# Kernel tuning notes

Measured on AMD Instinct MI355X. Metric: run time of the kernel, lower is better.

Reference implementation:

```python
import jax, jax.numpy as jnp
import numpy as np

IN_FEATURES = 4096
OUT_FEATURES = 16384
TOKENS = 8192  # batch 2 * seq 4096, flattened


def setup_inputs() -> dict:
    key = jax.random.key(0)
    k_x, k_w, k_s, k_b = jax.random.split(key, 4)
    x = jax.random.normal(k_x, (TOKENS, IN_FEATURES), dtype=jnp.float32)
    # ternary weights in {-1, 0, +1}, stored as low-precision ints
    weight_ternary = jax.random.randint(k_w, (OUT_FEATURES, IN_FEATURES), 0, 3, dtype=jnp.int32) - 1
    weight_scale = jax.random.uniform(k_s, (1,), dtype=jnp.float32) + 0.5
    bias = jax.random.normal(k_b, (OUT_FEATURES,), dtype=jnp.float32)
    return {"x": x, "weight_ternary": weight_ternary, "weight_scale": weight_scale, "bias": bias}


def reference(x, weight_ternary, weight_scale, bias):
    # forward: out = x @ (ternary.float() * scale).T + bias  (F.linear)
    w_float = weight_ternary.astype(jnp.float32) * weight_scale  # [O, I]
    out = jnp.einsum('ti,oi->to', x, w_float) + bias  # [T, O]
    return out
```

## Files before the change

kernel.cpp:

```cpp
#include <hip/hip_runtime.h>
#include <stdint.h>

#define TOKENS 8192
#define IN_F   4096
#define OUT_F  16384

#define BM 256
#define BN 256
#define BK 128
#define NT (IN_F / BK)

typedef __attribute__((ext_vector_type(4))) float f32x4;
typedef __attribute__((ext_vector_type(4))) int i32x4;


__device__ __forceinline__ int pack4(int a, int b, int c, int d) {
  return (a & 0xff) | ((b & 0xff) << 8) | ((c & 0xff) << 16) | ((d & 0xff) << 24);
}

__global__ void convert_w_i8(const int* __restrict__ w,
                             int8_t* __restrict__ wq, int n16) {
  int stride = gridDim.x * blockDim.x;
  for (int i = blockIdx.x * blockDim.x + threadIdx.x; i < n16; i += stride) {
    i32x4 o;
#pragma unroll
    for (int j = 0; j < 4; ++j) {
      i32x4 a = ((const i32x4*)w)[(size_t)i * 4 + j];
      o[j] = pack4(a.x, a.y, a.z, a.w);
    }
    ((i32x4*)wq)[i] = o;
  }
}

__global__ void convert_x_i8(const float* __restrict__ x,
                             int8_t* __restrict__ xq,
                             float* __restrict__ xs) {
  const int t = blockIdx.x;
  const int tid = threadIdx.x;
  const float* xr = x + (size_t)t * IN_F;

  f32x4 v[4];
  float m = 0.f;
#pragma unroll
  for (int i = 0; i < 4; ++i) {
    v[i] = ((const f32x4*)xr)[tid * 4 + i];
    m = fmaxf(m, fmaxf(fmaxf(fabsf(v[i].x), fabsf(v[i].y)),
                       fmaxf(fabsf(v[i].z), fabsf(v[i].w))));
  }
#pragma unroll
  for (int off = 32; off; off >>= 1) m = fmaxf(m, __shfl_xor(m, off));
  __shared__ float sm[4];
  if ((tid & 63) == 0) sm[tid >> 6] = m;
  __syncthreads();
  m = fmaxf(fmaxf(sm[0], sm[1]), fmaxf(sm[2], sm[3]));

  const float inv = (m > 0.f) ? (127.f / m) : 0.f;
  if (tid == 0) xs[t] = m / 127.f;

  i32x4 o;
#pragma unroll
  for (int i = 0; i < 4; ++i) {
    o[i] = pack4(__float2int_rn(v[i].x * inv), __float2int_rn(v[i].y * inv),
                 __float2int_rn(v[i].z * inv), __float2int_rn(v[i].w * inv));
  }
  ((i32x4*)(xq + (size_t)t * IN_F))[tid] = o;
}


__device__ __forceinline__ void async_lds_16B(const int8_t* g, int8_t* l) {
  __builtin_amdgcn_global_load_lds(
      reinterpret_cast<const __attribute__((address_space(1))) unsigned int*>(
          reinterpret_cast<uintptr_t>(g)),
      reinterpret_cast<__attribute__((address_space(3))) unsigned int*>(
          reinterpret_cast<uintptr_t>(l)),
      16, 0, 0);
}

__global__ __launch_bounds__(512, 2)
void ternary_gemm_i8(const int8_t* __restrict__ A,
                     const int8_t* __restrict__ B,
                     const float* __restrict__ xs,
                     const float* __restrict__ scale_p,
                     const float* __restrict__ bias,
                     float* __restrict__ C) {
  __shared__ __attribute__((aligned(16))) int8_t lds[2][2][BM * BK];

  const int nbn = OUT_F / BN;
  const int cpx = gridDim.x >> 3;
  const int bid = blockIdx.x;
  const int swz = (bid & 7) * cpx + (bid >> 3);
  const int bm = swz / nbn;
  const int bn = swz % nbn;

  const int tid  = threadIdx.x;
  const int lane = tid & 63;
  const int wid  = tid >> 6;
  const int wr   = wid >> 2;
  const int wc   = wid & 3;

  const int r = lane & 15;
  const int g = lane >> 4;
  const int swzr = (r & 7) * 16;

  const int8_t* Ag = A + (size_t)bm * BM * IN_F;
  const int8_t* Bg = B + (size_t)bn * BN * IN_F;

  const int s_rowoff = lane >> 3;
  const int s_colb   = ((lane & 7) ^ (lane >> 3)) * 16;

  auto stage = [&](int8_t* ldsTile, const int8_t* gTile, int half, int kt) {
#pragma unroll
    for (int i = 0; i < 2; ++i) {
      const int rbase = half * 128 + wid * 16 + i * 8;
      const int8_t* src =
          gTile + (size_t)(rbase + s_rowoff) * IN_F + kt * BK + s_colb;
      async_lds_16B(src, ldsTile + rbase * BK);
    }
  };

  i32x4 acc[8][4];
#pragma unroll
  for (int m = 0; m < 8; ++m)
#pragma unroll
    for (int n = 0; n < 4; ++n) acc[m][n] = i32x4{0, 0, 0, 0};

  stage(&lds[0][1][0], Bg, 0, 0);
  stage(&lds[0][1][0], Bg, 1, 0);
  stage(&lds[0][0][0], Ag, 0, 0);
  stage(&lds[0][0][0], Ag, 1, 0);
  stage(&lds[1][1][0], Bg, 0, 1);
  stage(&lds[1][1][0], Bg, 1, 1);
  stage(&lds[1][0][0], Ag, 0, 1);
  asm volatile("s_waitcnt vmcnt(6)" ::: "memory");
  __builtin_amdgcn_s_barrier();

  i32x4 bfr[4][2];
  i32x4 a0[2][2], a1[2][2], a2[2][2], a3[2][2];
#pragma unroll
  for (int n = 0; n < 4; ++n)
#pragma unroll
    for (int ks = 0; ks < 2; ++ks)
      bfr[n][ks] = *(const i32x4*)(&lds[0][1][0] + (wc * 64 + n * 16 + r) * BK +
                                   ((ks * 64 + g * 16) ^ swzr));
#pragma unroll
  for (int m = 0; m < 2; ++m)
#pragma unroll
    for (int ks = 0; ks < 2; ++ks)
      a0[m][ks] = *(const i32x4*)(&lds[0][0][0] + (wr * 128 + m * 16 + r) * BK +
                                  ((ks * 64 + g * 16) ^ swzr));
  asm volatile("s_waitcnt lgkmcnt(0)" ::: "memory");
  __builtin_amdgcn_s_barrier();

  for (int t = 0; t < NT; ++t) {
    const int cur = t & 1;
    const int8_t* Ab = &lds[cur][0][0];
    int8_t* Abw = &lds[cur][0][0];
    int8_t* Bbw = &lds[cur][1][0];
    int8_t* An  = &lds[cur ^ 1][0][0];
    const int8_t* AbN = &lds[cur ^ 1][0][0];
    const int8_t* BbN = &lds[cur ^ 1][1][0];

    __builtin_amdgcn_s_setprio(1);
#pragma unroll
    for (int ks = 0; ks < 2; ++ks)
#pragma unroll
      for (int m = 0; m < 2; ++m)
#pragma unroll
        for (int n = 0; n < 4; ++n)
          acc[m][n] = __builtin_amdgcn_mfma_i32_16x16x64_i8(
              a0[m][ks], bfr[n][ks], acc[m][n], 0, 0, 0);
    __builtin_amdgcn_s_setprio(0);
#pragma unroll
    for (int m = 0; m < 2; ++m)
#pragma unroll
      for (int ks = 0; ks < 2; ++ks)
        a1[m][ks] = *(const i32x4*)(Ab + (wr * 128 + (2 + m) * 16 + r) * BK +
                                    ((ks * 64 + g * 16) ^ swzr));
    if (t + 1 < NT) stage(An, Ag, 1, t + 1);

    __builtin_amdgcn_s_setprio(1);
#pragma unroll
    for (int ks = 0; ks < 2; ++ks)
#pragma unroll
      for (int m = 0; m < 2; ++m)
#pragma unroll
        for (int n = 0; n < 4; ++n)
          acc[2 + m][n] = __builtin_amdgcn_mfma_i32_16x16x64_i8(
              a1[m][ks], bfr[n][ks], acc[2 + m][n], 0, 0, 0);
    __builtin_amdgcn_s_setprio(0);
#pragma unroll
    for (int m = 0; m < 2; ++m)
#pragma unroll
      for (int ks = 0; ks < 2; ++ks)
        a2[m][ks] = *(const i32x4*)(Ab + (wr * 128 + (4 + m) * 16 + r) * BK +
                                    ((ks * 64 + g * 16) ^ swzr));
    if (t + 2 < NT) stage(Bbw, Bg, 0, t + 2);

    __builtin_amdgcn_s_setprio(1);
#pragma unroll
    for (int ks = 0; ks < 2; ++ks)
#pragma unroll
      for (int m = 0; m < 2; ++m)
#pragma unroll
        for (int n = 0; n < 4; ++n)
          acc[4 + m][n] = __builtin_amdgcn_mfma_i32_16x16x64_i8(
              a2[m][ks], bfr[n][ks], acc[4 + m][n], 0, 0, 0);
    __builtin_amdgcn_s_setprio(0);
#pragma unroll
    for (int m = 0; m < 2; ++m)
#pragma unroll
      for (int ks = 0; ks < 2; ++ks)
        a3[m][ks] = *(const i32x4*)(Ab + (wr * 128 + (6 + m) * 16 + r) * BK +
                                    ((ks * 64 + g * 16) ^ swzr));
    if (t + 2 < NT) stage(Bbw, Bg, 1, t + 2);
    asm volatile("s_waitcnt lgkmcnt(0)" ::: "memory");
    __builtin_amdgcn_s_barrier();

    __builtin_amdgcn_s_setprio(1);
#pragma unroll
    for (int ks = 0; ks < 2; ++ks)
#pragma unroll
      for (int m = 0; m < 2; ++m)
#pragma unroll
        for (int n = 0; n < 4; ++n)
          acc[6 + m][n] = __builtin_amdgcn_mfma_i32_16x16x64_i8(
              a3[m][ks], bfr[n][ks], acc[6 + m][n], 0, 0, 0);
    __builtin_amdgcn_s_setprio(0);
    if (t + 2 < NT) {
      stage(Abw, Ag, 0, t + 2);
      asm volatile("s_waitcnt vmcnt(6)" ::: "memory");
    } else {
      asm volatile("s_waitcnt vmcnt(0)" ::: "memory");
    }
    __builtin_amdgcn_s_barrier();
    if (t + 1 < NT) {
#pragma unroll
      for (int n = 0; n < 4; ++n)
#pragma unroll
        for (int ks = 0; ks < 2; ++ks)
          bfr[n][ks] = *(const i32x4*)(BbN + (wc * 64 + n * 16 + r) * BK +
                                       ((ks * 64 + g * 16) ^ swzr));
#pragma unroll
      for (int m = 0; m < 2; ++m)
#pragma unroll
        for (int ks = 0; ks < 2; ++ks)
          a0[m][ks] = *(const i32x4*)(AbN + (wr * 128 + m * 16 + r) * BK +
                                      ((ks * 64 + g * 16) ^ swzr));
      asm volatile("s_waitcnt lgkmcnt(0)" ::: "memory");
    }
    __builtin_amdgcn_s_barrier();
  }

  const float s = scale_p[0];
  const int row0 = bm * BM + wr * 128;
  const int col0 = bn * BN + wc * 64;
  float bv[4];
#pragma unroll
  for (int n = 0; n < 4; ++n) bv[n] = bias[col0 + n * 16 + r];
#pragma unroll
  for (int m = 0; m < 8; ++m) {
#pragma unroll
    for (int j = 0; j < 4; ++j) {
      const int row = row0 + m * 16 + g * 4 + j;
      const float sx = xs[row] * s;
#pragma unroll
      for (int n = 0; n < 4; ++n) {
        const int col = col0 + n * 16 + r;
        C[(size_t)row * OUT_F + col] = (float)acc[m][n][j] * sx + bv[n];
      }
    }
  }
}


__global__ void fallback_kernel(const float* __restrict__ x,
                                const int* __restrict__ w,
                                const float* __restrict__ scale_p,
                                const float* __restrict__ bias,
                                float* __restrict__ out) {
  size_t idx = (size_t)blockIdx.x * 256 + threadIdx.x;
  int t = (int)(idx / OUT_F);
  int o = (int)(idx % OUT_F);
  const float* xr = x + (size_t)t * IN_F;
  const int* wr = w + (size_t)o * IN_F;
  float acc = 0.f;
  for (int k = 0; k < IN_F; ++k) acc += xr[k] * (float)wr[k];
  out[idx] = acc * scale_p[0] + bias[o];
}


extern "C" void kernel_launch(void* const* d_in, const int* in_sizes, int n_in,
                              void* d_out, int out_size, void* d_ws, size_t ws_size,
                              hipStream_t stream) {
  const float* x     = (const float*)d_in[0];
  const int*   w     = (const int*)d_in[1];
  const float* scale = (const float*)d_in[2];
  const float* bias  = (const float*)d_in[3];
  float* out = (float*)d_out;

  const size_t wq_bytes = (size_t)OUT_F * IN_F;
  const size_t xq_bytes = (size_t)TOKENS * IN_F;
  const size_t xs_bytes = (size_t)TOKENS * sizeof(float);

  if (ws_size >= wq_bytes + xq_bytes + xs_bytes) {
    int8_t* wq = (int8_t*)d_ws;
    int8_t* xq = (int8_t*)((char*)d_ws + wq_bytes);
    float*  xs = (float*)((char*)d_ws + wq_bytes + xq_bytes);

    convert_w_i8<<<2048, 256, 0, stream>>>(w, wq, (OUT_F * IN_F) / 16);
    convert_x_i8<<<TOKENS, 256, 0, stream>>>(x, xq, xs);

    dim3 grid((TOKENS / BM) * (OUT_F / BN));
    ternary_gemm_i8<<<grid, 512, 0, stream>>>(xq, wq, xs, scale, bias, out);
  } else {
    size_t total = (size_t)TOKENS * OUT_F;
    fallback_kernel<<<(unsigned)(total / 256), 256, 0, stream>>>(x, w, scale, bias, out);
  }
}
```

Before: 622.6 us.

## Load B fragments directly from global into registers, bypassing LDS

The weight (B) tile is no longer staged through shared memory. Each wave now loads its own B fragments straight from global memory into registers after the last MFMA group of each k-step, and only the activation (A) tile stays double-buffered in LDS. This halves the LDS footprint and removes the B LDS writes and reads. In exchange, the two waves sharing a column slice each fetch the same B data, and the global load latency sits much closer to the point of use.

New measurement: 913.6 us. +46.7%, slower.

```diff
diff --git a/kernel.cpp b/kernel.cpp
--- a/kernel.cpp
+++ b/kernel.cpp
@@ -83,7 +83,7 @@
                      const float* __restrict__ scale_p,
                      const float* __restrict__ bias,
                      float* __restrict__ C) {
-  __shared__ __attribute__((aligned(16))) int8_t lds[2][2][BM * BK];
+  __shared__ __attribute__((aligned(16))) int8_t lds[2][BM * BK];
 
   const int nbn = OUT_F / BN;
   const int cpx = gridDim.x >> 3;
@@ -103,62 +103,62 @@
   const int swzr = (r & 7) * 16;
 
   const int8_t* Ag = A + (size_t)bm * BM * IN_F;
-  const int8_t* Bg = B + (size_t)bn * BN * IN_F;
+  const int8_t* Bg_lane =
+      B + (size_t)(bn * BN + wc * 64 + r) * IN_F + g * 16;
 
   const int s_rowoff = lane >> 3;
   const int s_colb   = ((lane & 7) ^ (lane >> 3)) * 16;
 
-  auto stage = [&](int8_t* ldsTile, const int8_t* gTile, int half, int kt) {
+  auto stageA = [&](int8_t* ldsTile, int half, int kt) {
 #pragma unroll
     for (int i = 0; i < 2; ++i) {
       const int rbase = half * 128 + wid * 16 + i * 8;
       const int8_t* src =
-          gTile + (size_t)(rbase + s_rowoff) * IN_F + kt * BK + s_colb;
+          Ag + (size_t)(rbase + s_rowoff) * IN_F + kt * BK + s_colb;
       async_lds_16B(src, ldsTile + rbase * BK);
     }
   };
 
+  auto loadB = [&](i32x4 (&bf)[4][2], int kt) {
+#pragma unroll
+    for (int n = 0; n < 4; ++n)
+#pragma unroll
+      for (int ks = 0; ks < 2; ++ks)
+        bf[n][ks] = *(const i32x4*)(Bg_lane + (size_t)(n * 16) * IN_F +
+                                    kt * BK + ks * 64);
+  };
+
   i32x4 acc[8][4];
 #pragma unroll
   for (int m = 0; m < 8; ++m)
 #pragma unroll
     for (int n = 0; n < 4; ++n) acc[m][n] = i32x4{0, 0, 0, 0};
-
-  stage(&lds[0][1][0], Bg, 0, 0);
-  stage(&lds[0][1][0], Bg, 1, 0);
-  stage(&lds[0][0][0], Ag, 0, 0);
-  stage(&lds[0][0][0], Ag, 1, 0);
-  stage(&lds[1][1][0], Bg, 0, 1);
-  stage(&lds[1][1][0], Bg, 1, 1);
-  stage(&lds[1][0][0], Ag, 0, 1);
-  asm volatile("s_waitcnt vmcnt(6)" ::: "memory");
-  __builtin_amdgcn_s_barrier();
 
   i32x4 bfr[4][2];
   i32x4 a0[2][2], a1[2][2], a2[2][2], a3[2][2];
-#pragma unroll
-  for (int n = 0; n < 4; ++n)
-#pragma unroll
-    for (int ks = 0; ks < 2; ++ks)
-      bfr[n][ks] = *(const i32x4*)(&lds[0][1][0] + (wc * 64 + n * 16 + r) * BK +
-                                   ((ks * 64 + g * 16) ^ swzr));
+
+  stageA(&lds[0][0], 0, 0);
+  stageA(&lds[0][0], 1, 0);
+  stageA(&lds[1][0], 0, 1);
+  loadB(bfr, 0);
+  asm volatile("s_waitcnt vmcnt(10)" ::: "memory");
+  __builtin_amdgcn_s_barrier();
+
 #pragma unroll
   for (int m = 0; m < 2; ++m)
 #pragma unroll
     for (int ks = 0; ks < 2; ++ks)
-      a0[m][ks] = *(const i32x4*)(&lds[0][0][0] + (wr * 128 + m * 16 + r) * BK +
+      a0[m][ks] = *(const i32x4*)(&lds[0][0] + (wr * 128 + m * 16 + r) * BK +
                                   ((ks * 64 + g * 16) ^ swzr));
   asm volatile("s_waitcnt lgkmcnt(0)" ::: "memory");
   __builtin_amdgcn_s_barrier();
 
   for (int t = 0; t < NT; ++t) {
     const int cur = t & 1;
-    const int8_t* Ab = &lds[cur][0][0];
-    int8_t* Abw = &lds[cur][0][0];
-    int8_t* Bbw = &lds[cur][1][0];
-    int8_t* An  = &lds[cur ^ 1][0][0];
-    const int8_t* AbN = &lds[cur ^ 1][0][0];
-    const int8_t* BbN = &lds[cur ^ 1][1][0];
+    const int8_t* Ab = &lds[cur][0];
+    int8_t* Abw = &lds[cur][0];
+    int8_t* An  = &lds[cur ^ 1][0];
+    const int8_t* AbN = &lds[cur ^ 1][0];
 
     __builtin_amdgcn_s_setprio(1);
 #pragma unroll
@@ -176,7 +176,7 @@
       for (int ks = 0; ks < 2; ++ks)
         a1[m][ks] = *(const i32x4*)(Ab + (wr * 128 + (2 + m) * 16 + r) * BK +
                                     ((ks * 64 + g * 16) ^ swzr));
-    if (t + 1 < NT) stage(An, Ag, 1, t + 1);
+    if (t + 1 < NT) stageA(An, 1, t + 1);
 
     __builtin_amdgcn_s_setprio(1);
 #pragma unroll
@@ -194,7 +194,6 @@
       for (int ks = 0; ks < 2; ++ks)
         a2[m][ks] = *(const i32x4*)(Ab + (wr * 128 + (4 + m) * 16 + r) * BK +
                                     ((ks * 64 + g * 16) ^ swzr));
-    if (t + 2 < NT) stage(Bbw, Bg, 0, t + 2);
 
     __builtin_amdgcn_s_setprio(1);
 #pragma unroll
@@ -212,7 +211,6 @@
       for (int ks = 0; ks < 2; ++ks)
         a3[m][ks] = *(const i32x4*)(Ab + (wr * 128 + (6 + m) * 16 + r) * BK +
                                     ((ks * 64 + g * 16) ^ swzr));
-    if (t + 2 < NT) stage(Bbw, Bg, 1, t + 2);
     asm volatile("s_waitcnt lgkmcnt(0)" ::: "memory");
     __builtin_amdgcn_s_barrier();
 
@@ -226,20 +224,15 @@
           acc[6 + m][n] = __builtin_amdgcn_mfma_i32_16x16x64_i8(
               a3[m][ks], bfr[n][ks], acc[6 + m][n], 0, 0, 0);
     __builtin_amdgcn_s_setprio(0);
+    if (t + 1 < NT) loadB(bfr, t + 1);
     if (t + 2 < NT) {
-      stage(Abw, Ag, 0, t + 2);
-      asm volatile("s_waitcnt vmcnt(6)" ::: "memory");
+      stageA(Abw, 0, t + 2);
+      asm volatile("s_waitcnt vmcnt(10)" ::: "memory");
     } else {
       asm volatile("s_waitcnt vmcnt(0)" ::: "memory");
     }
     __builtin_amdgcn_s_barrier();
     if (t + 1 < NT) {
-#pragma unroll
-      for (int n = 0; n < 4; ++n)
-#pragma unroll
-        for (int ks = 0; ks < 2; ++ks)
-          bfr[n][ks] = *(const i32x4*)(BbN + (wc * 64 + n * 16 + r) * BK +
-                                       ((ks * 64 + g * 16) ^ swzr));
 #pragma unroll
       for (int m = 0; m < 2; ++m)
 #pragma unroll
```
